# Optimization experiments

Hardware: AMD Instinct MI355X
Metric: run time of the kernel (lower is better)

The kernel has to match this reference:

```python
import jax, jax.numpy as jnp
import numpy as np

BN_EPS = 1e-5
LEAKY_SLOPE = 0.01
DK = 64


def setup_inputs() -> dict:
    key = jax.random.key(0)
    ks = jax.random.split(key, 9)
    B, N, C = 8, 2048, 256
    H, dk, dv = 8, 64, 64
    return {
        "x": jax.random.normal(ks[0], (B, N, C), jnp.float32),
        "Wq": jax.random.normal(ks[1], (H, dk, C), jnp.float32) * (1.0 / np.sqrt(C)),
        "Wk": jax.random.normal(ks[2], (H, dk, C), jnp.float32) * (1.0 / np.sqrt(C)),
        "Wv": jax.random.normal(ks[3], (H, dv, C), jnp.float32) * (1.0 / np.sqrt(C)),
        "Wp": jax.random.normal(ks[4], (C, H * dv), jnp.float32) * (1.0 / np.sqrt(H * dv)),
        "bn_gamma": jax.random.uniform(ks[5], (C,), jnp.float32, 0.5, 1.5),
        "bn_beta": jax.random.normal(ks[6], (C,), jnp.float32) * 0.1,
        "bn_mean": jax.random.normal(ks[7], (C,), jnp.float32) * 0.1,
        "bn_var": jax.random.uniform(ks[8], (C,), jnp.float32, 0.5, 1.5),
    }


def reference(x, Wq, Wk, Wv, Wp, bn_gamma, bn_beta, bn_mean, bn_var):
    # x: [B,N,C]; per-head 1x1 Conv1d projections batched over heads h.
    q = jnp.einsum("bnc,hkc->bhnk", x, Wq)   # [B,H,N,dk]
    k = jnp.einsum("bnc,hkc->bhnk", x, Wk)   # [B,H,N,dk]
    v = jnp.einsum("bnc,hvc->bhnv", x, Wv)   # [B,H,N,dv]
    energy = jnp.einsum("bhnk,bhmk->bhnm", q, k)  # [B,H,N,N]
    scale = 1.0 / jnp.sqrt(jnp.float32(DK))
    attn = jax.nn.softmax(energy * scale, axis=-1)
    xw = jnp.einsum("bhnm,bhmv->bhnv", attn, v)   # [B,H,N,dv]
    # torch.cat(heads, dim=2) -> [B,N,H*dv] with head-major ordering
    B, H, N, dv = xw.shape
    cat = jnp.transpose(xw, (0, 2, 1, 3)).reshape(B, N, H * dv)
    # LBRD: 1x1 conv (no bias) + BatchNorm1d (inference stats) + LeakyReLU + Dropout(0)
    y = jnp.einsum("bnf,cf->bnc", cat, Wp)
    y = (y - bn_mean) * (bn_gamma * jax.lax.rsqrt(bn_var + BN_EPS)) + bn_beta
    y = jnp.where(y >= 0, y, LEAKY_SLOPE * y)
    return y
```

## Files before the change

kernel.cpp:

```cpp
#include <hip/hip_runtime.h>
#include <hip/hip_bf16.h>

typedef unsigned short u16;
typedef unsigned int u32;
typedef float  f32x4 __attribute__((ext_vector_type(4)));
typedef short  s16x8 __attribute__((ext_vector_type(8)));

#define DEV static __device__ __forceinline__

DEV u16 f2bf(float f){ union{float f; unsigned int i;} c; c.f=f; unsigned int i=c.i;
                       return (u16)((i + 0x7FFFu + ((i>>16)&1u))>>16); }

DEV u32 pkbf(float a, float b){
  union{ __hip_bfloat162 h; u32 u; } c;
  c.h = __float22bfloat162_rn(make_float2(a, b));
  return c.u;
}

DEV float exp2a(float x){
#if __has_builtin(__builtin_amdgcn_exp2f)
  return __builtin_amdgcn_exp2f(x);
#else
  return exp2f(x);
#endif
}

DEV s16x8 ld_frag(const u16* p){
  union{ s16x8 v; uint2 u[2]; } r;
  r.u[0] = *(const uint2*)(p);
  r.u[1] = *(const uint2*)(p+16);
  return r.v;
}

DEV s16x8 ld_frag_f32(const float* p){
  float4 a = *(const float4*)(p);
  float4 b = *(const float4*)(p+16);
  union{ s16x8 v; u32 u[4]; } r;
  r.u[0]=pkbf(a.x,a.y); r.u[1]=pkbf(a.z,a.w);
  r.u[2]=pkbf(b.x,b.y); r.u[3]=pkbf(b.z,b.w);
  return r.v;
}

__global__ __launch_bounds__(256) void cvt_w_kernel(
    const float* __restrict__ w0, const float* __restrict__ w1,
    const float* __restrict__ w2, const float* __restrict__ w3,
    u16* __restrict__ d0, u16* __restrict__ d1,
    u16* __restrict__ d2, u16* __restrict__ d3)
{
  const int z = blockIdx.y;
  const float* src = (z==0)?w0:(z==1)?w1:(z==2)?w2:w3;
  u16* dst = (z==0)?d0:(z==1)?d1:(z==2)?d2:d3;
  int i = blockIdx.x*256 + threadIdx.x;
  if (i >= 32768) return;
  float4 v = *(const float4*)(src + (size_t)i*4);
  ushort4 o;
  o.x = f2bf(v.x); o.y = f2bf(v.y); o.z = f2bf(v.z); o.w = f2bf(v.w);
  *(ushort4*)(dst + (size_t)i*4) = o;
}

__global__ __launch_bounds__(256) void kv_kernel(
    const float* __restrict__ x32, const u16* __restrict__ Wk,
    const u16* __restrict__ Wv, u16* __restrict__ kbuf, u16* __restrict__ vbuf)
{
  const int isV = blockIdx.z;
  const u16* W = isV ? Wv : Wk;
  const int m0 = blockIdx.x*64, j0 = blockIdx.y*64;
  __shared__ u16 at[64][40];
  __shared__ u16 bt[64][40];
  const int tid = threadIdx.x, lane = tid&63, w = tid>>6;
  const int wm = w>>1, wn = w&1;
  const int l16 = lane&15, lq = lane>>4;
  f32x4 acc[2][2] = {};
  const int srow = tid>>2, scol = (tid&3)*8;
  for (int c0=0;c0<256;c0+=32){
    {
      const float* xs = x32 + (size_t)(m0+srow)*256 + c0 + scol;
      float4 a = *(const float4*)xs;
      float4 b = *(const float4*)(xs+4);
      uint4 st; st.x=pkbf(a.x,a.y); st.y=pkbf(a.z,a.w); st.z=pkbf(b.x,b.y); st.w=pkbf(b.z,b.w);
      *(uint4*)&at[srow][scol] = st;
    }
    *(uint4*)&bt[srow][scol] = *(const uint4*)&W[(size_t)(j0+srow)*256 + c0 + scol];
    __syncthreads();
    s16x8 af[2], bfr[2];
    #pragma unroll
    for(int mf=0;mf<2;mf++) af[mf]  = ld_frag(&at[wm*32+mf*16+l16][lq*4]);
    #pragma unroll
    for(int nf=0;nf<2;nf++) bfr[nf] = ld_frag(&bt[wn*32+nf*16+l16][lq*4]);
    #pragma unroll
    for(int mf=0;mf<2;mf++)
      #pragma unroll
      for(int nf=0;nf<2;nf++)
        acc[mf][nf] = __builtin_amdgcn_mfma_f32_16x16x32_bf16(af[mf], bfr[nf], acc[mf][nf],0,0,0);
    __syncthreads();
  }
  if (!isV){
    #pragma unroll
    for(int mf=0;mf<2;mf++)
      #pragma unroll
      for(int nf=0;nf<2;nf++){
        const int j  = j0 + wn*32 + nf*16 + l16;
        const int hh = j>>6;
        const int kkp = wn*32 + (l16>>2)*8 + nf*4 + (l16&3);
        #pragma unroll
        for(int r=0;r<4;r++){
          int m = m0 + wm*32 + mf*16 + lq*4 + r;
          int blx = m>>11, n = m&2047;
          kbuf[(size_t)((blx<<3)|hh)*131072 + (size_t)n*64 + kkp] = f2bf(acc[mf][nf][r]);
        }
      }
  } else {
    const int blx = m0>>11;
    #pragma unroll
    for(int mf=0;mf<2;mf++){
      const int nn = (m0&2047) + wm*32 + lq*8 + mf*4;
      #pragma unroll
      for(int nf=0;nf<2;nf++){
        const int j  = j0 + wn*32 + nf*16 + l16;
        const int hh = j>>6, kk = j&63;
        uint2 st;
        st.x = pkbf(acc[mf][nf][0], acc[mf][nf][1]);
        st.y = pkbf(acc[mf][nf][2], acc[mf][nf][3]);
        *(uint2*)&vbuf[(size_t)((blx<<3)|hh)*131072 + (size_t)kk*2048 + nn] = st;
      }
    }
  }
}

__global__ __launch_bounds__(256) void attn_kernel(
    const float* __restrict__ x32, const u16* __restrict__ Wq,
    const u16* __restrict__ kb, const u16* __restrict__ vb,
    u16* __restrict__ cat, int bh_per_xcd)
{
  const int lin = blockIdx.x;
  const int xcd = lin & 7, slot = lin >> 3;
  const int bhl = xcd*bh_per_xcd + (slot>>4);
  const int n0  = (slot & 15) * 128;
  const int bl = bhl>>3, h = bhl&7;
  const float* xg = x32 + (size_t)bl*524288;
  const u16* kg = kb + (size_t)bhl*131072;
  const u16* vg = vb + (size_t)bhl*131072;
  u16* catp = cat + (size_t)bl*1048576 + h*64;
  const int tid=threadIdx.x, lane=tid&63, w=tid>>6;
  const int l16=lane&15, lq=lane>>4;

  __shared__ __align__(16) u16 kt[64][72];
  __shared__ __align__(16) u16 vt[64][72];

  s16x8 qf[2][2];
  {
    const u16* wqh = Wq + (size_t)h*16384;
    s16x8 xf[2][8];
    #pragma unroll
    for(int sub=0;sub<2;sub++){
      const int row = n0 + w*32 + sub*16 + l16;
      #pragma unroll
      for(int kc8=0;kc8<8;kc8++)
        xf[sub][kc8] = ld_frag_f32(xg + (size_t)row*256 + kc8*32 + lq*4);
    }
    f32x4 dq[2][4] = {};
    #pragma unroll
    for(int df=0;df<4;df++)
      #pragma unroll
      for(int kc8=0;kc8<8;kc8++){
        s16x8 wf = ld_frag(wqh + (size_t)(df*16+l16)*256 + kc8*32 + lq*4);
        dq[0][df] = __builtin_amdgcn_mfma_f32_16x16x32_bf16(wf, xf[0][kc8], dq[0][df],0,0,0);
        dq[1][df] = __builtin_amdgcn_mfma_f32_16x16x32_bf16(wf, xf[1][kc8], dq[1][df],0,0,0);
      }
    const float SCL = 0.125f * 1.44269504088896f;
    #pragma unroll
    for(int sub=0;sub<2;sub++)
      #pragma unroll
      for(int kc=0;kc<2;kc++){
        union{s16x8 v; u32 u[4];} t;
        t.u[0]=pkbf(dq[sub][2*kc][0]*SCL,  dq[sub][2*kc][1]*SCL);
        t.u[1]=pkbf(dq[sub][2*kc][2]*SCL,  dq[sub][2*kc][3]*SCL);
        t.u[2]=pkbf(dq[sub][2*kc+1][0]*SCL,dq[sub][2*kc+1][1]*SCL);
        t.u[3]=pkbf(dq[sub][2*kc+1][2]*SCL,dq[sub][2*kc+1][3]*SCL);
        qf[sub][kc]=t.v;
      }
  }

  s16x8 ones;
  #pragma unroll
  for(int e=0;e<8;e++) ones[e] = (short)0x3F80;

  const int srow = tid>>2, sc = (tid&3)*16;
  const u16* kst = kg + (size_t)srow*64 + sc;
  const u16* vst = vg + (size_t)srow*2048 + sc;
  uint4 kr0,kr1,vr0,vr1;
  kr0 = *(const uint4*)(kst);   kr1 = *(const uint4*)(kst+8);
  vr0 = *(const uint4*)(vst);   vr1 = *(const uint4*)(vst+8);
  *(uint4*)&kt[srow][sc] = kr0;  *(uint4*)&kt[srow][sc+8] = kr1;
  *(uint4*)&vt[srow][sc] = vr0;  *(uint4*)&vt[srow][sc+8] = vr1;
  kr0 = *(const uint4*)(kst + 4096);  kr1 = *(const uint4*)(kst + 4096 + 8);
  vr0 = *(const uint4*)(vst + 64);    vr1 = *(const uint4*)(vst + 64 + 8);
  __syncthreads();

  f32x4 oacc[2][4] = {};
  f32x4 accl[2] = {};

  for(int t=0;t<32;t++){
    s16x8 kf[8], vf[8];
    #pragma unroll
    for(int jf=0;jf<4;jf++)
      #pragma unroll
      for(int kc=0;kc<2;kc++)
        kf[jf*2+kc] = *(const s16x8*)&kt[jf*16+l16][kc*32+lq*8];
    #pragma unroll
    for(int cf=0;cf<4;cf++)
      #pragma unroll
      for(int kc=0;kc<2;kc++)
        vf[cf*2+kc] = *(const s16x8*)&vt[cf*16+l16][kc*32+lq*8];

    if (t<31){
      __syncthreads();
      *(uint4*)&kt[srow][sc]   = kr0;  *(uint4*)&kt[srow][sc+8] = kr1;
      *(uint4*)&vt[srow][sc]   = vr0;  *(uint4*)&vt[srow][sc+8] = vr1;
      if (t<30){
        kr0 = *(const uint4*)(kst + (size_t)(t+2)*4096);
        kr1 = *(const uint4*)(kst + (size_t)(t+2)*4096 + 8);
        vr0 = *(const uint4*)(vst + (size_t)(t+2)*64);
        vr1 = *(const uint4*)(vst + (size_t)(t+2)*64 + 8);
      }
    }

    f32x4 sacc[2][4] = {};
    #pragma unroll
    for(int jf=0;jf<4;jf++)
      #pragma unroll
      for(int kc=0;kc<2;kc++){
        sacc[0][jf]=__builtin_amdgcn_mfma_f32_16x16x32_bf16(kf[jf*2+kc],qf[0][kc],sacc[0][jf],0,0,0);
        sacc[1][jf]=__builtin_amdgcn_mfma_f32_16x16x32_bf16(kf[jf*2+kc],qf[1][kc],sacc[1][jf],0,0,0);
      }
    s16x8 pf[2][2];
    #pragma unroll
    for(int sub=0;sub<2;sub++)
      #pragma unroll
      for(int kc=0;kc<2;kc++){
        union{s16x8 v; u32 u[4];} tt;
        tt.u[0]=pkbf(exp2a(sacc[sub][2*kc][0]),  exp2a(sacc[sub][2*kc][1]));
        tt.u[1]=pkbf(exp2a(sacc[sub][2*kc][2]),  exp2a(sacc[sub][2*kc][3]));
        tt.u[2]=pkbf(exp2a(sacc[sub][2*kc+1][0]),exp2a(sacc[sub][2*kc+1][1]));
        tt.u[3]=pkbf(exp2a(sacc[sub][2*kc+1][2]),exp2a(sacc[sub][2*kc+1][3]));
        pf[sub][kc]=tt.v;
      }
    #pragma unroll
    for(int kc=0;kc<2;kc++){
      accl[0]=__builtin_amdgcn_mfma_f32_16x16x32_bf16(ones,pf[0][kc],accl[0],0,0,0);
      accl[1]=__builtin_amdgcn_mfma_f32_16x16x32_bf16(ones,pf[1][kc],accl[1],0,0,0);
    }
    #pragma unroll
    for(int cf=0;cf<4;cf++)
      #pragma unroll
      for(int kc=0;kc<2;kc++){
        oacc[0][cf]=__builtin_amdgcn_mfma_f32_16x16x32_bf16(vf[cf*2+kc],pf[0][kc],oacc[0][cf],0,0,0);
        oacc[1][cf]=__builtin_amdgcn_mfma_f32_16x16x32_bf16(vf[cf*2+kc],pf[1][kc],oacc[1][cf],0,0,0);
      }
    if (t<31) __syncthreads();
  }
  #pragma unroll
  for(int sub=0;sub<2;sub++){
    const float rinv = 1.f/accl[sub][0];
    const int n = n0 + w*32 + sub*16 + l16;
    #pragma unroll
    for(int cf=0;cf<4;cf++){
      uint2 st;
      st.x = pkbf(oacc[sub][cf][0]*rinv, oacc[sub][cf][1]*rinv);
      st.y = pkbf(oacc[sub][cf][2]*rinv, oacc[sub][cf][3]*rinv);
      *(uint2*)(catp + (size_t)n*512 + cf*16 + lq*4) = st;
    }
  }
}

__global__ __launch_bounds__(256) void proj_kernel(
    const u16* __restrict__ cat, const u16* __restrict__ Wp,
    const float* __restrict__ gamma, const float* __restrict__ beta,
    const float* __restrict__ mean,  const float* __restrict__ var,
    float* __restrict__ out)
{
  const int m0 = blockIdx.x*64, j0 = blockIdx.y*64;
  __shared__ u16 at[64][40];
  __shared__ u16 bt[64][40];
  const int tid=threadIdx.x, lane=tid&63, w=tid>>6;
  const int wm=w>>1, wn=w&1, l16=lane&15, lq=lane>>4;
  f32x4 acc[2][2]={};
  const int srow=tid>>2, scol=(tid&3)*8;
  for(int c0=0;c0<512;c0+=32){
    *(uint4*)&at[srow][scol] = *(const uint4*)&cat[(size_t)(m0+srow)*512 + c0+scol];
    *(uint4*)&bt[srow][scol] = *(const uint4*)&Wp[(size_t)(j0+srow)*512 + c0+scol];
    __syncthreads();
    s16x8 af[2],bfr[2];
    #pragma unroll
    for(int mf=0;mf<2;mf++) af[mf]=ld_frag(&at[wm*32+mf*16+l16][lq*4]);
    #pragma unroll
    for(int nf=0;nf<2;nf++) bfr[nf]=ld_frag(&bt[wn*32+nf*16+l16][lq*4]);
    #pragma unroll
    for(int mf=0;mf<2;mf++)
      #pragma unroll
      for(int nf=0;nf<2;nf++)
        acc[mf][nf]=__builtin_amdgcn_mfma_f32_16x16x32_bf16(af[mf],bfr[nf],acc[mf][nf],0,0,0);
    __syncthreads();
  }
  #pragma unroll
  for(int nf=0;nf<2;nf++){
    const int co = j0 + wn*32 + nf*16 + l16;
    const float g=gamma[co], be=beta[co], mu=mean[co], va=var[co];
    const float a  = g * rsqrtf(va + 1e-5f);
    const float b2 = be - mu*a;
    #pragma unroll
    for(int mf=0;mf<2;mf++)
      #pragma unroll
      for(int r=0;r<4;r++){
        int m = m0 + wm*32 + mf*16 + lq*4 + r;
        float y = acc[mf][nf][r]*a + b2;
        y = (y>=0.f)? y : 0.01f*y;
        out[(size_t)m*256 + co] = y;
      }
  }
}

extern "C" void kernel_launch(void* const* d_in, const int* in_sizes, int n_in,
                              void* d_out, int out_size, void* d_ws, size_t ws_size,
                              hipStream_t stream)
{
  const float* x  = (const float*)d_in[0];
  const float* Wq = (const float*)d_in[1];
  const float* Wk = (const float*)d_in[2];
  const float* Wv = (const float*)d_in[3];
  const float* Wp = (const float*)d_in[4];
  const float* g  = (const float*)d_in[5];
  const float* be = (const float*)d_in[6];
  const float* mu = (const float*)d_in[7];
  const float* va = (const float*)d_in[8];

  u16* ws   = (u16*)d_ws;
  u16* wq16 = ws;
  u16* wk16 = ws + 131072;
  u16* wv16 = ws + 262144;
  u16* wp16 = ws + 393216;
  u16* kb   = ws + 524288;

  cvt_w_kernel<<<dim3(128,4), 256, 0, stream>>>(Wq, Wk, Wv, Wp, wq16, wk16, wv16, wp16);

  const size_t full_elems = 524288ull + 8388608ull*3ull;
  if (ws_size >= full_elems*2ull){
    u16* vb  = kb + 8388608;
    u16* cat = vb + 8388608;
    kv_kernel<<<dim3(256,8,2), dim3(256), 0, stream>>>(x, wk16, wv16, kb, vb);
    attn_kernel<<<dim3(1024), dim3(256), 0, stream>>>(x, wq16, kb, vb, cat, 8);
    proj_kernel<<<dim3(256,4), dim3(256), 0, stream>>>(cat, wp16, g, be, mu, va, (float*)d_out);
  } else {
    u16* vb  = kb + 4194304;
    u16* cat = vb + 4194304;
    for (int half = 0; half < 2; ++half){
      const float* xh = x + (size_t)half*2097152;
      u16* cath = cat + (size_t)half*4194304;
      kv_kernel<<<dim3(128,8,2), dim3(256), 0, stream>>>(xh, wk16, wv16, kb, vb);
      attn_kernel<<<dim3(512), dim3(256), 0, stream>>>(xh, wq16, kb, vb, cath, 4);
    }
    proj_kernel<<<dim3(256,4), dim3(256), 0, stream>>>(cat, wp16, g, be, mu, va, (float*)d_out);
  }
}
```

Measured before the change: 172.0 us.

## Stream K/V tiles via direct global-to-LDS loads with XOR swizzle and double buffering

Replaces the register-staged K/V tile loads in the attention loop with global_load_lds direct-to-LDS copies into a double-buffered shared tile. The padded layout is replaced by an XOR swizzle applied when the projection kernel writes K and V, so LDS fragment reads stay bank-conflict-free without padding. This removes the VGPR staging and the extra LDS store instructions. The visible part of the loop no longer has the mid-iteration barrier, so correctness depends on a sync and wait for the async loads existing in the unseen remainder of the loop.

```diff
diff --git a/kernel.cpp b/kernel.cpp
--- a/kernel.cpp
+++ b/kernel.cpp
@@ -23,6 +23,12 @@
 #else
   return exp2f(x);
 #endif
+}
+
+typedef const __attribute__((address_space(1))) void* gas1p;
+typedef __attribute__((address_space(3))) void* las3p;
+DEV void gll16(const void* g, void* l){
+  __builtin_amdgcn_global_load_lds((gas1p)g, (las3p)l, 16, 0, 0);
 }
 
 DEV s16x8 ld_frag(const u16* p){
@@ -106,18 +112,20 @@
         for(int r=0;r<4;r++){
           int m = m0 + wm*32 + mf*16 + lq*4 + r;
           int blx = m>>11, n = m&2047;
-          kbuf[(size_t)((blx<<3)|hh)*131072 + (size_t)n*64 + kkp] = f2bf(acc[mf][nf][r]);
+          const int kkx = kkp ^ ((n&7)<<3);
+          kbuf[(size_t)((blx<<3)|hh)*131072 + (size_t)n*64 + kkx] = f2bf(acc[mf][nf][r]);
         }
       }
   } else {
     const int blx = m0>>11;
     #pragma unroll
     for(int mf=0;mf<2;mf++){
-      const int nn = (m0&2047) + wm*32 + lq*8 + mf*4;
+      const int nnw = wm*32 + lq*8 + mf*4;
       #pragma unroll
       for(int nf=0;nf<2;nf++){
         const int j  = j0 + wn*32 + nf*16 + l16;
         const int hh = j>>6, kk = j&63;
+        const int nn = (m0&2047) + (nnw ^ ((l16&7)<<3));
         uint2 st;
         st.x = pkbf(acc[mf][nf][0], acc[mf][nf][1]);
         st.y = pkbf(acc[mf][nf][2], acc[mf][nf][3]);
@@ -144,8 +152,8 @@
   const int tid=threadIdx.x, lane=tid&63, w=tid>>6;
   const int l16=lane&15, lq=lane>>4;
 
-  __shared__ __align__(16) u16 kt[64][72];
-  __shared__ __align__(16) u16 vt[64][72];
+  __shared__ __align__(16) u16 kt[2][64][64];
+  __shared__ __align__(16) u16 vt[2][64][64];
 
   s16x8 qf[2][2];
   {
@@ -185,45 +193,47 @@
   #pragma unroll
   for(int e=0;e<8;e++) ones[e] = (short)0x3F80;
 
-  const int srow = tid>>2, sc = (tid&3)*16;
-  const u16* kst = kg + (size_t)srow*64 + sc;
-  const u16* vst = vg + (size_t)srow*2048 + sc;
-  uint4 kr0,kr1,vr0,vr1;
-  kr0 = *(const uint4*)(kst);   kr1 = *(const uint4*)(kst+8);
-  vr0 = *(const uint4*)(vst);   vr1 = *(const uint4*)(vst+8);
-  *(uint4*)&kt[srow][sc] = kr0;  *(uint4*)&kt[srow][sc+8] = kr1;
-  *(uint4*)&vt[srow][sc] = vr0;  *(uint4*)&vt[srow][sc+8] = vr1;
-  kr0 = *(const uint4*)(kst + 4096);  kr1 = *(const uint4*)(kst + 4096 + 8);
-  vr0 = *(const uint4*)(vst + 64);    vr1 = *(const uint4*)(vst + 64 + 8);
+  const int ldsw  = w<<10;
+  const int myoff = ldsw + (lane<<4);
+  const char* kgb = (const char*)kg;
+  const char* vgb = (const char*)vg;
+  char* ktb = (char*)&kt[0][0][0];
+  char* vtb = (char*)&vt[0][0][0];
+  const int off0 = myoff, off1 = 4096 + myoff;
+  const size_t voff0 = (size_t)(off0>>7)*4096 + (off0&127);
+  const size_t voff1 = (size_t)(off1>>7)*4096 + (off1&127);
+
+  gll16(kgb + myoff,        ktb + ldsw);
+  gll16(kgb + 4096 + myoff, ktb + 4096 + ldsw);
+  gll16(vgb + voff0,        vtb + ldsw);
+  gll16(vgb + voff1,        vtb + 4096 + ldsw);
   __syncthreads();
 
+  const int xsw = (l16&7)<<3;
   f32x4 oacc[2][4] = {};
   f32x4 accl[2] = {};
 
   for(int t=0;t<32;t++){
+    const int cur = t&1, nb = cur^1;
+    if (t<31){
+      const size_t kofs = (size_t)(t+1)*8192;
+      const size_t vofs = (size_t)(t+1)*128;
+      gll16(kgb + kofs + myoff,        ktb + nb*8192 + ldsw);
+      gll16(kgb + kofs + 4096 + myoff, ktb + nb*8192 + 4096 + ldsw);
+      gll16(vgb + voff0 + vofs,        vtb + nb*8192 + ldsw);
+      gll16(vgb + voff1 + vofs,        vtb + nb*8192 + 4096 + ldsw);
+    }
     s16x8 kf[8], vf[8];
     #pragma unroll
     for(int jf=0;jf<4;jf++)
       #pragma unroll
       for(int kc=0;kc<2;kc++)
-        kf[jf*2+kc] = *(const s16x8*)&kt[jf*16+l16][kc*32+lq*8];
+        kf[jf*2+kc] = *(const s16x8*)&kt[cur][jf*16+l16][(kc*32+lq*8) ^ xsw];
     #pragma unroll
     for(int cf=0;cf<4;cf++)
       #pragma unroll
       for(int kc=0;kc<2;kc++)
-        vf[cf*2+kc] = *(const s16x8*)&vt[cf*16+l16][kc*32+lq*8];
-
-    if (t<31){
-      __syncthreads();
-      *(uint4*)&kt[srow][sc]   = kr0;  *(uint4*)&kt[srow][sc+8] = kr1;
-      *(uint4*)&vt[srow][sc]   = vr0;  *(uint4*)&vt[srow][sc+8] = vr1;
-      if (t<30){
-        kr0 = *(const uint4*)(kst + (size_t)(t+2)*4096);
-        kr1 = *(const uint4*)(kst + (size_t)(t+2)*4096 + 8);
-        vr0 = *(const uint4*)(vst + (size_t)(t+2)*64);
-        vr1 = *(const uint4*)(vst + (size_t)(t+2)*64 + 8);
-      }
-    }
+        vf[cf*2+kc] = *(const s16x8*)&vt[cur][cf*16+l16][(kc*32+lq*8) ^ xsw];
 
     f32x4 sacc[2][4] = {};
     #pragma unroll
```

After: 192.7 us. 12.0% more time.
